# Kernel tuning notes

Measured on AMD Instinct MI355X. Metric: run time of the kernel, lower is better.

The kernel has to match this reference:

```python
import jax, jax.numpy as jnp
import numpy as np


def setup_inputs() -> dict:
    key = jax.random.key(0)
    ks = jax.random.split(key, 4)
    B, N, C, S, D_AGG, D_OUT = 16, 2048, 128, 25, 128, 128
    # sparse binary adjacency, avg degree ~ N*0.01 ~ 20
    A = (jax.random.uniform(ks[0], (B, N, N)) < 0.01).astype(jnp.float32)
    X = jax.random.normal(ks[1], (B, N, C), dtype=jnp.float32)
    Wa = jax.random.normal(ks[2], (C, D_AGG), dtype=jnp.float32) * 0.05
    ba = jnp.zeros((D_AGG,), jnp.float32)
    Wc = jax.random.normal(ks[3], (C + D_AGG, D_OUT), dtype=jnp.float32) * 0.05
    bc = jnp.zeros((D_OUT,), jnp.float32)
    return {"A": A, "X": X, "Wa": Wa, "ba": ba, "Wc": Wc, "bc": bc, "n_samples": S}


def reference(A, X, Wa, ba, Wc, bc, n_samples):
    # Per node: take up to n_samples neighbors (nonzero adjacency entries).
    # Original randomly subsamples when degree > S; we take the first S by
    # index (lax.top_k is stable, ties -> lowest index). Missing slots are
    # zero rows, matching the original tf.pad: they contribute relu(ba) to
    # the max-aggregator, exactly like the padded/no-neighbor branches.
    mask = (A != 0).astype(X.dtype)                      # [B,N,N]
    vals, idx = jax.lax.top_k(mask, n_samples)           # [B,N,S]
    feats = jax.vmap(lambda x, i: jnp.take(x, i, axis=0))(X, idx)  # [B,N,S,C]
    feats = feats * vals[..., None]                      # zero padded slots
    # max aggregator: relu(neigh @ Wa + ba), max over sampled neighbors
    h = jax.nn.relu(jnp.einsum('bnsc,cd->bnsd', feats, Wa) + ba)
    agg = h.max(axis=2)                                  # [B,N,D_AGG]
    # concat self features with aggregated, project, relu
    cat = jnp.concatenate([X, agg], axis=-1)             # [B,N,C+D_AGG]
    out = jax.nn.relu(jnp.einsum('bnk,ko->bno', cat, Wc) + bc)  # [B,N,D_OUT]
    # per-graph Frobenius-norm normalization with div_no_nan semantics
    norm = jnp.sqrt(jnp.sum(out * out, axis=(1, 2), keepdims=True))
    return jnp.where(norm > 0, out / norm, jnp.zeros_like(out))
```

## Files before the change

kernel.cpp:

```cpp
#include <hip/hip_runtime.h>


typedef __attribute__((ext_vector_type(8))) short short8;
typedef __attribute__((ext_vector_type(4))) float f32x4;
typedef __attribute__((ext_vector_type(4))) float fvec4;
typedef unsigned int uint;
typedef unsigned short ushort;

__device__ __forceinline__ ushort f2bf(float x) {
    uint u = __builtin_bit_cast(uint, x);
    u += 0x7FFFu + ((u >> 16) & 1u);
    return (ushort)(u >> 16);
}
__device__ __forceinline__ float bflo(uint h) { uint v = h << 16;         return __builtin_bit_cast(float, v); }
__device__ __forceinline__ float bfhi(uint h) { uint v = h & 0xFFFF0000u; return __builtin_bit_cast(float, v); }

__global__ __launch_bounds__(256) void prep_w_k(
    const float* __restrict__ Wa, const float* __restrict__ Wc,
    ushort* __restrict__ Wat, ushort* __restrict__ Wct)
{
    int i = blockIdx.x * 256 + threadIdx.x;
    if (i < 16384) {
        int d = i >> 7, k = i & 127;
        Wat[i] = f2bf(Wa[k * 128 + d]);
    } else {
        int j = i - 16384;
        int d = j >> 8, k = j & 255;
        Wct[j] = f2bf(Wc[k * 128 + d]);
    }
}

__global__ __launch_bounds__(256) void gemm_mfma_k(
    const float*  __restrict__ Xf,
    const ushort* __restrict__ A1,
    const ushort* __restrict__ Bt,
    const float*  __restrict__ bias,
    ushort* __restrict__ outH,
    float*  __restrict__ outF,
    float*  __restrict__ partials,
    int ktiles)
{
    __shared__ ushort Asm[128 * 128];
    __shared__ ushort Bsm[128 * 128];
    __shared__ float wred[4];
    const int tid = threadIdx.x;
    const int l = tid & 63, w = tid >> 6;
    const int wm = (w >> 1) * 64, wn = (w & 1) * 64;
    const size_t row0 = (size_t)blockIdx.x * 128;
    const int KT = ktiles << 7;

    f32x4 acc[4][4] = {};

    for (int t = 0; t < ktiles; ++t) {
        __syncthreads();
        if (t == 0) {
#pragma unroll
            for (int j = 0; j < 8; ++j) {
                int gid = (j << 8) + tid;
                int r = gid >> 4, g = gid & 15;
                const float* s = Xf + (row0 + r) * 128 + g * 8;
                short8 pk;
#pragma unroll
                for (int e = 0; e < 8; ++e) pk[e] = (short)f2bf(s[e]);
                *(short8*)&Asm[r * 128 + ((g ^ (r & 7)) << 3)] = pk;
            }
        } else {
#pragma unroll
            for (int j = 0; j < 8; ++j) {
                int gid = (j << 8) + tid;
                int r = gid >> 4, g = gid & 15;
                short8 v = *(const short8*)(A1 + (row0 + r) * 128 + g * 8);
                *(short8*)&Asm[r * 128 + ((g ^ (r & 7)) << 3)] = v;
            }
        }
#pragma unroll
        for (int j = 0; j < 8; ++j) {
            int gid = (j << 8) + tid;
            int r = gid >> 4, g = gid & 15;
            short8 v = *(const short8*)(Bt + (size_t)r * KT + (t << 7) + g * 8);
            *(short8*)&Bsm[r * 128 + ((g ^ (r & 7)) << 3)] = v;
        }
        __syncthreads();
#pragma unroll
        for (int ks = 0; ks < 4; ++ks) {
            int gg = (ks << 2) + (l >> 4);
            short8 af[4], bfr[4];
#pragma unroll
            for (int m = 0; m < 4; ++m) {
                int r = wm + m * 16 + (l & 15);
                af[m] = *(const short8*)&Asm[r * 128 + ((gg ^ (r & 7)) << 3)];
            }
#pragma unroll
            for (int n = 0; n < 4; ++n) {
                int c = wn + n * 16 + (l & 15);
                bfr[n] = *(const short8*)&Bsm[c * 128 + ((gg ^ (c & 7)) << 3)];
            }
#pragma unroll
            for (int m = 0; m < 4; ++m)
#pragma unroll
                for (int n = 0; n < 4; ++n)
                    acc[m][n] = __builtin_amdgcn_mfma_f32_16x16x32_bf16(
                        af[m], bfr[n], acc[m][n], 0, 0, 0);
        }
    }

    float bcol[4];
#pragma unroll
    for (int n = 0; n < 4; ++n) bcol[n] = bias[wn + n * 16 + (l & 15)];
    float lsum = 0.f;
#pragma unroll
    for (int m = 0; m < 4; ++m) {
        int rbase = wm + m * 16 + ((l >> 4) << 2);
#pragma unroll
        for (int n = 0; n < 4; ++n) {
            int col = wn + n * 16 + (l & 15);
#pragma unroll
            for (int r = 0; r < 4; ++r) {
                float v = fmaxf(acc[m][n][r] + bcol[n], 0.f);
                size_t o = (row0 + rbase + r) * 128 + col;
                if (outH) outH[o] = f2bf(v);
                else { outF[o] = v; lsum += v * v; }
            }
        }
    }
    if (partials) {
#pragma unroll
        for (int off = 32; off > 0; off >>= 1) lsum += __shfl_down(lsum, off);
        if (l == 0) wred[w] = lsum;
        __syncthreads();
        if (tid == 0) partials[blockIdx.x] = wred[0] + wred[1] + wred[2] + wred[3];
    }
}

__global__ __launch_bounds__(256) void agg_k(
    const float* __restrict__ A,
    const uint*  __restrict__ Hu,
    const float* __restrict__ ba,
    uint* __restrict__ aggu,
    const int* __restrict__ nsp)
{
    __shared__ int idxs[4][32];
    const int l = threadIdx.x & 63;
    const int w = threadIdx.x >> 6;
    const int node = blockIdx.x * 4 + w;
    const int b = node >> 11;
    int S = nsp[0]; if (S > 32) S = 32;

    const fvec4* rowp = (const fvec4*)(A + (size_t)node * 2048);
    fvec4 v[8];
#pragma unroll
    for (int c = 0; c < 8; ++c)
        v[c] = __builtin_nontemporal_load(rowp + c * 64 + l);

    int found = 0;
#pragma unroll
    for (int c = 0; c < 8; ++c) {
        if (found >= S) break;
        unsigned long long m0 = __ballot(v[c][0] != 0.f);
        unsigned long long m1 = __ballot(v[c][1] != 0.f);
        unsigned long long m2 = __ballot(v[c][2] != 0.f);
        unsigned long long m3 = __ballot(v[c][3] != 0.f);
        unsigned long long any = m0 | m1 | m2 | m3;
        while (any && found < S) {
            int bl = __builtin_ctzll(any);
            any &= any - 1;
            unsigned long long bit = 1ull << bl;
            int e = (c << 8) + (bl << 2);
            if ((m0 & bit) && found < S) { if (l == 0) idxs[w][found] = e;     ++found; }
            if ((m1 & bit) && found < S) { if (l == 0) idxs[w][found] = e + 1; ++found; }
            if ((m2 & bit) && found < S) { if (l == 0) idxs[w][found] = e + 2; ++found; }
            if ((m3 & bit) && found < S) { if (l == 0) idxs[w][found] = e + 3; ++found; }
        }
    }

    float i0 = fmaxf(ba[2 * l], 0.f), i1 = fmaxf(ba[2 * l + 1], 0.f);
    float a0[4] = {i0, i0, i0, i0}, a1[4] = {i1, i1, i1, i1};
    const uint* HB = Hu + ((size_t)b << 17);
    int j = 0;
    for (; j + 4 <= found; j += 4) {
        int n0 = idxs[w][j], n1 = idxs[w][j + 1];
        int n2 = idxs[w][j + 2], n3 = idxs[w][j + 3];
        uint h0 = HB[(size_t)n0 * 64 + l];
        uint h1 = HB[(size_t)n1 * 64 + l];
        uint h2 = HB[(size_t)n2 * 64 + l];
        uint h3 = HB[(size_t)n3 * 64 + l];
        a0[0] = fmaxf(a0[0], bflo(h0)); a1[0] = fmaxf(a1[0], bfhi(h0));
        a0[1] = fmaxf(a0[1], bflo(h1)); a1[1] = fmaxf(a1[1], bfhi(h1));
        a0[2] = fmaxf(a0[2], bflo(h2)); a1[2] = fmaxf(a1[2], bfhi(h2));
        a0[3] = fmaxf(a0[3], bflo(h3)); a1[3] = fmaxf(a1[3], bfhi(h3));
    }
    for (; j < found; ++j) {
        uint h = HB[(size_t)idxs[w][j] * 64 + l];
        a0[0] = fmaxf(a0[0], bflo(h)); a1[0] = fmaxf(a1[0], bfhi(h));
    }
    float r0 = fmaxf(fmaxf(a0[0], a0[1]), fmaxf(a0[2], a0[3]));
    float r1 = fmaxf(fmaxf(a1[0], a1[1]), fmaxf(a1[2], a1[3]));
    aggu[(size_t)node * 64 + l] = (uint)f2bf(r0) | ((uint)f2bf(r1) << 16);
}

__global__ __launch_bounds__(256) void scale_k(
    float* __restrict__ out, const float* __restrict__ partials)
{
    const int blk = blockIdx.x;
    const int b = blk >> 6;
    float s = 0.f;
#pragma unroll
    for (int i = 0; i < 16; ++i) s += partials[b * 16 + i];
    float norm = sqrtf(s);
    float sc = (norm > 0.f) ? (1.f / norm) : 0.f;
    fvec4* o4 = (fvec4*)out;
    int i0 = blk * 1024 + threadIdx.x;
#pragma unroll
    for (int k = 0; k < 4; ++k) {
        fvec4 v = o4[i0 + k * 256];
        o4[i0 + k * 256] = v * sc;
    }
}

extern "C" void kernel_launch(void* const* d_in, const int* in_sizes, int n_in,
                              void* d_out, int out_size, void* d_ws, size_t ws_size,
                              hipStream_t stream) {
    const float* A  = (const float*)d_in[0];
    const float* X  = (const float*)d_in[1];
    const float* Wa = (const float*)d_in[2];
    const float* ba = (const float*)d_in[3];
    const float* Wc = (const float*)d_in[4];
    const float* bc = (const float*)d_in[5];
    const int*  nsp = (const int*)d_in[6];

    float* out = (float*)d_out;
    char* ws = (char*)d_ws;
    ushort* H        = (ushort*)ws;
    ushort* agg      = (ushort*)(ws + (8u << 20));
    ushort* Wat      = (ushort*)(ws + (16u << 20));
    ushort* Wct      = (ushort*)(ws + (16u << 20) + 32768);
    float*  partials = (float*) (ws + (16u << 20) + 131072);

    prep_w_k<<<192, 256, 0, stream>>>(Wa, Wc, Wat, Wct);
    gemm_mfma_k<<<256, 256, 0, stream>>>(X, nullptr, Wat, ba, H, nullptr, nullptr, 1);
    agg_k<<<8192, 256, 0, stream>>>(A, (const uint*)H, ba, (uint*)agg, nsp);
    gemm_mfma_k<<<256, 256, 0, stream>>>(X, agg, Wct, bc, nullptr, out, partials, 2);
    scale_k<<<1024, 256, 0, stream>>>(out, partials);
}
```

Baseline: 97.14 us.

## Parallelize neighbor index compaction via ballot prefix counts and widen gather loop

Replaces the serial per-bit loop that collected neighbor indices with a parallel compaction, where every lane computes its rank from ballot masks and popcounts. The gather loop is widened to 8 independent loads per round, with the index list padded by repeating a valid neighbor, which leaves the max unchanged. The Wc transpose is moved out of the prep kernel and into extra blocks of the aggregation kernel. The aim is to cut serial scalar work and raise memory-level parallelism in the gather, since the kernel is bound by its 256MB adjacency read.

Result: faster. 93.42 us (-3.8%).

```diff
diff --git a/kernel.cpp b/kernel.cpp
--- a/kernel.cpp
+++ b/kernel.cpp
@@ -16,18 +16,11 @@
 __device__ __forceinline__ float bfhi(uint h) { uint v = h & 0xFFFF0000u; return __builtin_bit_cast(float, v); }
 
 __global__ __launch_bounds__(256) void prep_w_k(
-    const float* __restrict__ Wa, const float* __restrict__ Wc,
-    ushort* __restrict__ Wat, ushort* __restrict__ Wct)
+    const float* __restrict__ Wa, ushort* __restrict__ Wat)
 {
     int i = blockIdx.x * 256 + threadIdx.x;
-    if (i < 16384) {
-        int d = i >> 7, k = i & 127;
-        Wat[i] = f2bf(Wa[k * 128 + d]);
-    } else {
-        int j = i - 16384;
-        int d = j >> 8, k = j & 255;
-        Wct[j] = f2bf(Wc[k * 128 + d]);
-    }
+    int d = i >> 7, k = i & 127;
+    Wat[i] = f2bf(Wa[k * 128 + d]);
 }
 
 __global__ __launch_bounds__(256) void gemm_mfma_k(
@@ -137,8 +130,17 @@
     const uint*  __restrict__ Hu,
     const float* __restrict__ ba,
     uint* __restrict__ aggu,
-    const int* __restrict__ nsp)
-{
+    const int* __restrict__ nsp,
+    const float* __restrict__ Wc,
+    ushort* __restrict__ Wct)
+{
+    if (blockIdx.x >= 8192) {
+        int j = (blockIdx.x - 8192) * 256 + threadIdx.x;
+        int d = j >> 8, k = j & 255;
+        Wct[j] = f2bf(Wc[k * 128 + d]);
+        return;
+    }
+
     __shared__ int idxs[4][32];
     const int l = threadIdx.x & 63;
     const int w = threadIdx.x >> 6;
@@ -152,50 +154,67 @@
     for (int c = 0; c < 8; ++c)
         v[c] = __builtin_nontemporal_load(rowp + c * 64 + l);
 
-    int found = 0;
+    const unsigned long long lt = (1ull << l) - 1ull;
+    int base = 0;
 #pragma unroll
     for (int c = 0; c < 8; ++c) {
-        if (found >= S) break;
-        unsigned long long m0 = __ballot(v[c][0] != 0.f);
-        unsigned long long m1 = __ballot(v[c][1] != 0.f);
-        unsigned long long m2 = __ballot(v[c][2] != 0.f);
-        unsigned long long m3 = __ballot(v[c][3] != 0.f);
-        unsigned long long any = m0 | m1 | m2 | m3;
-        while (any && found < S) {
-            int bl = __builtin_ctzll(any);
-            any &= any - 1;
-            unsigned long long bit = 1ull << bl;
-            int e = (c << 8) + (bl << 2);
-            if ((m0 & bit) && found < S) { if (l == 0) idxs[w][found] = e;     ++found; }
-            if ((m1 & bit) && found < S) { if (l == 0) idxs[w][found] = e + 1; ++found; }
-            if ((m2 & bit) && found < S) { if (l == 0) idxs[w][found] = e + 2; ++found; }
-            if ((m3 & bit) && found < S) { if (l == 0) idxs[w][found] = e + 3; ++found; }
-        }
-    }
+        if (base < S) {
+            unsigned long long m0 = __ballot(v[c][0] != 0.f);
+            unsigned long long m1 = __ballot(v[c][1] != 0.f);
+            unsigned long long m2 = __ballot(v[c][2] != 0.f);
+            unsigned long long m3 = __ballot(v[c][3] != 0.f);
+            int below = __popcll(m0 & lt) + __popcll(m1 & lt)
+                      + __popcll(m2 & lt) + __popcll(m3 & lt);
+            int o0 = (int)((m0 >> l) & 1), o1 = (int)((m1 >> l) & 1);
+            int o2 = (int)((m2 >> l) & 1), o3 = (int)((m3 >> l) & 1);
+            int r0 = base + below;
+            int r1 = r0 + o0, r2 = r1 + o1, r3 = r2 + o2;
+            int e = (c << 8) + (l << 2);
+            if (o0 && r0 < S) idxs[w][r0] = e;
+            if (o1 && r1 < S) idxs[w][r1] = e + 1;
+            if (o2 && r2 < S) idxs[w][r2] = e + 2;
+            if (o3 && r3 < S) idxs[w][r3] = e + 3;
+            base += __popcll(m0) + __popcll(m1) + __popcll(m2) + __popcll(m3);
+        }
+    }
+    int found = base < S ? base : S;
 
     float i0 = fmaxf(ba[2 * l], 0.f), i1 = fmaxf(ba[2 * l + 1], 0.f);
-    float a0[4] = {i0, i0, i0, i0}, a1[4] = {i1, i1, i1, i1};
-    const uint* HB = Hu + ((size_t)b << 17);
-    int j = 0;
-    for (; j + 4 <= found; j += 4) {
-        int n0 = idxs[w][j], n1 = idxs[w][j + 1];
-        int n2 = idxs[w][j + 2], n3 = idxs[w][j + 3];
-        uint h0 = HB[(size_t)n0 * 64 + l];
-        uint h1 = HB[(size_t)n1 * 64 + l];
-        uint h2 = HB[(size_t)n2 * 64 + l];
-        uint h3 = HB[(size_t)n3 * 64 + l];
-        a0[0] = fmaxf(a0[0], bflo(h0)); a1[0] = fmaxf(a1[0], bfhi(h0));
-        a0[1] = fmaxf(a0[1], bflo(h1)); a1[1] = fmaxf(a1[1], bfhi(h1));
-        a0[2] = fmaxf(a0[2], bflo(h2)); a1[2] = fmaxf(a1[2], bfhi(h2));
-        a0[3] = fmaxf(a0[3], bflo(h3)); a1[3] = fmaxf(a1[3], bfhi(h3));
-    }
-    for (; j < found; ++j) {
-        uint h = HB[(size_t)idxs[w][j] * 64 + l];
-        a0[0] = fmaxf(a0[0], bflo(h)); a1[0] = fmaxf(a1[0], bfhi(h));
-    }
-    float r0 = fmaxf(fmaxf(a0[0], a0[1]), fmaxf(a0[2], a0[3]));
-    float r1 = fmaxf(fmaxf(a1[0], a1[1]), fmaxf(a1[2], a1[3]));
-    aggu[(size_t)node * 64 + l] = (uint)f2bf(r0) | ((uint)f2bf(r1) << 16);
+    float r0f, r1f;
+    if (found > 0) {
+        int fill = idxs[w][0];
+        if (l < 32) {
+            int val = (l < found) ? idxs[w][l] : fill;
+            idxs[w][l] = val;
+        }
+        int rounds = (found + 7) >> 3;
+        float a0[8], a1[8];
+#pragma unroll
+        for (int q = 0; q < 8; ++q) { a0[q] = i0; a1[q] = i1; }
+        const uint* HB = Hu + ((size_t)b << 17);
+        for (int rr = 0; rr < rounds; ++rr) {
+            int jb = rr << 3;
+            uint h[8];
+#pragma unroll
+            for (int q = 0; q < 8; ++q)
+                h[q] = HB[(size_t)idxs[w][jb + q] * 64 + l];
+#pragma unroll
+            for (int q = 0; q < 8; ++q) {
+                a0[q] = fmaxf(a0[q], bflo(h[q]));
+                a1[q] = fmaxf(a1[q], bfhi(h[q]));
+            }
+        }
+#pragma unroll
+        for (int q = 0; q < 4; ++q) {
+            a0[q] = fmaxf(a0[q], a0[q + 4]);
+            a1[q] = fmaxf(a1[q], a1[q + 4]);
+        }
+        r0f = fmaxf(fmaxf(a0[0], a0[1]), fmaxf(a0[2], a0[3]));
+        r1f = fmaxf(fmaxf(a1[0], a1[1]), fmaxf(a1[2], a1[3]));
+    } else {
+        r0f = i0; r1f = i1;
+    }
+    aggu[(size_t)node * 64 + l] = (uint)f2bf(r0f) | ((uint)f2bf(r1f) << 16);
 }
 
 __global__ __launch_bounds__(256) void scale_k(
@@ -236,9 +255,9 @@
     ushort* Wct      = (ushort*)(ws + (16u << 20) + 32768);
     float*  partials = (float*) (ws + (16u << 20) + 131072);
 
-    prep_w_k<<<192, 256, 0, stream>>>(Wa, Wc, Wat, Wct);
+    prep_w_k<<<64, 256, 0, stream>>>(Wa, Wat);
     gemm_mfma_k<<<256, 256, 0, stream>>>(X, nullptr, Wat, ba, H, nullptr, nullptr, 1);
-    agg_k<<<8192, 256, 0, stream>>>(A, (const uint*)H, ba, (uint*)agg, nsp);
+    agg_k<<<8192 + 128, 256, 0, stream>>>(A, (const uint*)H, ba, (uint*)agg, nsp, Wc, Wct);
     gemm_mfma_k<<<256, 256, 0, stream>>>(X, agg, Wct, bc, nullptr, out, partials, 2);
     scale_k<<<1024, 256, 0, stream>>>(out, partials);
 }
```
